# Kernel optimization log

Measured on AMD Instinct MI355X. Metric: run time of the kernel, lower is better.

Reference implementation:

```python
import jax, jax.numpy as jnp
import numpy as np
from jax import lax

L = 6        # n_layers
C = 192      # hidden_channels
FC = 768     # filter_channels
H = 2        # n_heads
DK = C // H  # k_channels per head
K = 3        # ffn kernel_size
W = 4        # window_size
B = 4
T = 2048
EPS = 1e-5


def setup_inputs() -> dict:
    key = jax.random.key(0)
    ks = jax.random.split(key, 16)
    def rn(k, shape, scale):
        return jax.random.normal(k, shape, dtype=jnp.float32) * scale
    xavier = (2.0 / (C + C)) ** 0.5
    return {
        "x": jax.random.normal(ks[0], (B, C, T), dtype=jnp.float32),
        "x_mask": jnp.ones((B, 1, T), dtype=jnp.float32),
        "wq": rn(ks[1], (L, C, C), xavier), "bq": jnp.zeros((L, C), jnp.float32),
        "wk": rn(ks[2], (L, C, C), xavier), "bk": jnp.zeros((L, C), jnp.float32),
        "wv": rn(ks[3], (L, C, C), xavier), "bv": jnp.zeros((L, C), jnp.float32),
        "wo": rn(ks[4], (L, C, C), xavier), "bo": jnp.zeros((L, C), jnp.float32),
        "rel_k": rn(ks[5], (L, 1, 2 * W + 1, DK), DK ** -0.5),
        "rel_v": rn(ks[6], (L, 1, 2 * W + 1, DK), DK ** -0.5),
        "ln1_g": jnp.ones((L, C), jnp.float32), "ln1_b": jnp.zeros((L, C), jnp.float32),
        "ffn_w1": rn(ks[7], (L, FC, C, K), 0.02), "ffn_b1": jnp.zeros((L, FC), jnp.float32),
        "ffn_w2": rn(ks[8], (L, C, FC, K), 0.02), "ffn_b2": jnp.zeros((L, C), jnp.float32),
        "ln2_g": jnp.ones((L, C), jnp.float32), "ln2_b": jnp.zeros((L, C), jnp.float32),
    }


def _layer_norm_ch(x, g, b):
    # normalize over channel dim (axis=1) of [B, C, T]
    m = jnp.mean(x, axis=1, keepdims=True)
    v = jnp.mean((x - m) ** 2, axis=1, keepdims=True)
    return g[None, :, None] * (x - m) * lax.rsqrt(v + EPS) + b[None, :, None]


def _conv1x1(x, w, b):
    return jnp.einsum('oc,bct->bot', w, x) + b[None, :, None]


def _conv1d(x, w, b, pad):
    y = lax.conv_general_dilated(x, w, window_strides=(1,), padding=[(pad, pad)],
                                 dimension_numbers=('NCH', 'OIH', 'NCH'))
    return y + b[None, :, None]


def _get_rel(emb, length):
    # emb: [1, 2W+1, DK] -> [1, 2*length-1, DK]
    pad_len = max(length - (W + 1), 0)
    start = max(W + 1 - length, 0)
    emb = jnp.pad(emb, ((0, 0), (pad_len, pad_len), (0, 0)))
    return emb[:, start:start + 2 * length - 1]


def _rel_to_abs(x):
    # [B, H, L, 2L-1] -> [B, H, L, L]
    b, h, l, _ = x.shape
    x = jnp.pad(x, ((0, 0), (0, 0), (0, 0), (0, 1)))
    x = x.reshape(b, h, l * 2 * l)
    x = jnp.pad(x, ((0, 0), (0, 0), (0, l - 1)))
    return x.reshape(b, h, l + 1, 2 * l - 1)[:, :, :l, l - 1:]


def _abs_to_rel(x):
    # [B, H, L, L] -> [B, H, L, 2L-1]
    b, h, l, _ = x.shape
    x = jnp.pad(x, ((0, 0), (0, 0), (0, 0), (0, l - 1)))
    x = x.reshape(b, h, l * (2 * l - 1))
    x = jnp.pad(x, ((0, 0), (0, 0), (l, 0)))
    return x.reshape(b, h, l, 2 * l)[:, :, :, 1:]


def reference(x, x_mask, wq, bq, wk, bk, wv, bv, wo, bo, rel_k, rel_v,
              ln1_g, ln1_b, ffn_w1, ffn_b1, ffn_w2, ffn_b2, ln2_g, ln2_b):
    attn_mask = x_mask[:, :, None, :] * x_mask[:, :, :, None]  # [B,1,T,T]
    x = x * x_mask
    scale = DK ** -0.5
    pad = (K - 1) // 2
    for l in range(L):
        residual = x
        q = _conv1x1(x, wq[l], bq[l]).reshape(B, H, DK, T).transpose(0, 1, 3, 2)
        k = _conv1x1(x, wk[l], bk[l]).reshape(B, H, DK, T).transpose(0, 1, 3, 2)
        v = _conv1x1(x, wv[l], bv[l]).reshape(B, H, DK, T).transpose(0, 1, 3, 2)
        qs = q * scale
        scores = jnp.einsum('bhtd,bhsd->bhts', qs, k)
        rk = _get_rel(rel_k[l], T)[0]  # [2T-1, DK], heads shared
        scores = scores + _rel_to_abs(jnp.einsum('bhtd,md->bhtm', qs, rk))
        scores = jnp.where(attn_mask == 0, jnp.float32(-1e4), scores)
        p = jax.nn.softmax(scores, axis=-1)
        out = jnp.einsum('bhts,bhsd->bhtd', p, v)
        rv = _get_rel(rel_v[l], T)[0]
        out = out + jnp.einsum('bhtm,md->bhtd', _abs_to_rel(p), rv)
        out = out.transpose(0, 1, 3, 2).reshape(B, C, T)
        out = _conv1x1(out, wo[l], bo[l])
        x = _layer_norm_ch(residual + out, ln1_g[l], ln1_b[l])
        residual = x
        h = _conv1d(x * x_mask, ffn_w1[l], ffn_b1[l], pad)
        h = jax.nn.relu(h)  # activation != 'gelu'
        h = _conv1d(h, ffn_w2[l], ffn_b2[l], pad)
        h = h * x_mask
        x = _layer_norm_ch(residual + h, ln2_g[l], ln2_b[l])
    return x * x_mask
```

## Files before the change

kernel.cpp:

```cpp
#include <hip/hip_runtime.h>

#define LNUM 6
#define CH 192
#define FCH 768
#define NH 2
#define DKH 96
#define WIN 4
#define BATCH 4
#define TLEN 2048
#define EPSV 1e-5f
#define SCH 4
#define CHUNK (TLEN / SCH)
#define NBCT (BATCH*CH*TLEN)
#define NBFT (BATCH*FCH*TLEN)
#define BHT (BATCH*NH*TLEN)

typedef __attribute__((ext_vector_type(8))) short bf16x8;
typedef __attribute__((ext_vector_type(4))) float f32x4;
typedef __attribute__((ext_vector_type(8))) unsigned short u16x8;

__device__ __forceinline__ unsigned short f2bf(float f) {
  unsigned int u = __builtin_bit_cast(unsigned int, f);
  u = (u + 0x7fffu + ((u >> 16) & 1u)) >> 16;
  return (unsigned short)u;
}
__device__ __forceinline__ float bf2f(unsigned short s) {
  return __builtin_bit_cast(float, ((unsigned int)s) << 16);
}
__device__ __forceinline__ float exp2a(float x) {
#if __has_builtin(__builtin_amdgcn_exp2f)
  return __builtin_amdgcn_exp2f(x);
#else
  return exp2f(x);
#endif
}

__global__ __launch_bounds__(256) void prep_all(
    const float* __restrict__ wq, const float* __restrict__ wk, const float* __restrict__ wv,
    const float* __restrict__ bq, const float* __restrict__ bk, const float* __restrict__ bv,
    const float* __restrict__ wo, const float* __restrict__ fw1, const float* __restrict__ fw2,
    unsigned short* __restrict__ Wqkv, float* __restrict__ Bqkv,
    unsigned short* __restrict__ Wob, unsigned short* __restrict__ W1b,
    unsigned short* __restrict__ W2b)
{
  const float qscale = 0.10206207261596575f * 1.4426950408889634f;
  const int n0 = LNUM * 576 * CH;
  const int n1 = LNUM * CH * CH;
  const int n2 = LNUM * 3 * FCH * CH;
  const int n3 = LNUM * 3 * CH * FCH;
  int total = n0 + n1 + n2 + n3;
  for (int i = blockIdx.x * 256 + threadIdx.x; i < total; i += gridDim.x * 256) {
    if (i < n0) {
      int c = i % CH; int n = (i / CH) % 576; int l = i / (CH * 576);
      float sc = (n < 192) ? qscale : 1.f;
      const float* src = (n < 192) ? wq : (n < 384) ? wk : wv;
      int nn = n % 192;
      Wqkv[i] = f2bf(src[((size_t)l * CH + nn) * CH + c] * sc);
      if (c == 0) {
        const float* bs = (n < 192) ? bq : (n < 384) ? bk : bv;
        Bqkv[l * 576 + n] = bs[l * CH + nn] * sc;
      }
    } else if (i < n0 + n1) {
      int j = i - n0;
      Wob[j] = f2bf(wo[j]);
    } else if (i < n0 + n1 + n2) {
      int j = i - n0 - n1;
      int c = j % CH; int t1 = j / CH;
      int f = t1 % FCH; int t2 = t1 / FCH;
      int kk = t2 % 3; int l = t2 / 3;
      W1b[j] = f2bf(fw1[(((size_t)l * FCH + f) * CH + c) * 3 + kk]);
    } else {
      int j = i - n0 - n1 - n2;
      int c = j % FCH; int t1 = j / FCH;
      int f = t1 % CH; int t2 = t1 / CH;
      int kk = t2 % 3; int l = t2 / 3;
      W2b[j] = f2bf(fw2[(((size_t)l * CH + f) * FCH + c) * 3 + kk]);
    }
  }
}

__global__ __launch_bounds__(256) void tin_kernel(const float* __restrict__ x,
    const float* __restrict__ mask, float* __restrict__ Xc, unsigned short* __restrict__ Xbf) {
  __shared__ float ls[32][33];
  int b = blockIdx.z; int c0 = blockIdx.y * 32, t0 = blockIdx.x * 32;
  int tx = threadIdx.x & 31, ty = threadIdx.x >> 5;
  #pragma unroll
  for (int j = 0; j < 4; ++j)
    ls[ty + j * 8][tx] = x[((size_t)b * CH + c0 + ty + j * 8) * TLEN + t0 + tx];
  __syncthreads();
  #pragma unroll
  for (int j = 0; j < 4; ++j) {
    int t = t0 + ty + j * 8;
    float v = ls[tx][ty + j * 8] * mask[b * TLEN + t];
    size_t o = ((size_t)b * TLEN + t) * CH + c0 + tx;
    Xc[o] = v; Xbf[o] = f2bf(v);
  }
}

__global__ __launch_bounds__(256) void tout_kernel(const float* __restrict__ Xc,
    const float* __restrict__ mask, float* __restrict__ out) {
  __shared__ float ls[32][33];
  int b = blockIdx.z; int c0 = blockIdx.y * 32, t0 = blockIdx.x * 32;
  int tx = threadIdx.x & 31, ty = threadIdx.x >> 5;
  #pragma unroll
  for (int j = 0; j < 4; ++j)
    ls[ty + j * 8][tx] = Xc[((size_t)b * TLEN + t0 + ty + j * 8) * CH + c0 + tx];
  __syncthreads();
  #pragma unroll
  for (int j = 0; j < 4; ++j)
    out[((size_t)b * CH + c0 + ty + j * 8) * TLEN + t0 + tx] =
        ls[tx][ty + j * 8] * mask[b * TLEN + t0 + tx];
}

template<int OUTMODE, int NSHIFT, int RELU, int KSPLIT, int MFR>
__global__ __launch_bounds__(256) void gemm_tc(
    const unsigned short* __restrict__ A, const unsigned short* __restrict__ Bw,
    const float* __restrict__ bias, void* __restrict__ Y, int Cin, int N)
{
  constexpr int HALO = (NSHIFT == 3) ? 1 : 0;
  constexpr int AROWS = MFR * 32 + 2 * HALO;
  constexpr int ACH = (AROWS * 8 + 255) / 256;
  constexpr int BCH = (NSHIFT * 64 * 8) / 256;
  __shared__ __align__(16) unsigned short As[AROWS][72];
  __shared__ __align__(16) unsigned short Bs[NSHIFT][64][72];
  int zz = blockIdx.z;
  int b = zz / KSPLIT, ks = zz % KSPLIT;
  int t0 = blockIdx.x * (MFR * 32), n0 = blockIdx.y * 64;
  int tid = threadIdx.x;
  int w = tid >> 6, lane = tid & 63;
  int wr = w >> 1, wc = w & 1;
  int lr = lane & 15, lg = lane >> 4;
  const unsigned short* Ab = A + (size_t)b * TLEN * Cin;
  int klen = Cin / KSPLIT, k0 = ks * klen;

  int ar[ACH], ac8[ACH]; bool aok[ACH], ain[ACH];
  #pragma unroll
  for (int j = 0; j < ACH; ++j) {
    int f = tid + j * 256;
    ar[j] = f >> 3; ac8[j] = (f & 7) * 8;
    aok[j] = (f < AROWS * 8);
    int tg = t0 - HALO + ar[j];
    ain[j] = aok[j] && (!HALO || (tg >= 0 && tg < TLEN));
  }
  int brr[BCH], bkk[BCH], bc8[BCH];
  #pragma unroll
  for (int j = 0; j < BCH; ++j) {
    int f = tid + j * 256;
    bkk[j] = f >> 9; brr[j] = (f >> 3) & 63; bc8[j] = (f & 7) * 8;
  }

  u16x8 areg[ACH], breg[BCH];
  f32x4 acc[MFR][2] = {};

  #pragma unroll
  for (int j = 0; j < ACH; ++j) {
    u16x8 v = {};
    if (ain[j]) v = *(const u16x8*)&Ab[(size_t)(t0 - HALO + ar[j]) * Cin + k0 + ac8[j]];
    areg[j] = v;
  }
  #pragma unroll
  for (int j = 0; j < BCH; ++j)
    breg[j] = *(const u16x8*)&Bw[((size_t)bkk[j] * N + n0 + brr[j]) * Cin + k0 + bc8[j]];

  for (int kc = k0; kc < k0 + klen; kc += 64) {
    __syncthreads();
    #pragma unroll
    for (int j = 0; j < ACH; ++j)
      if (aok[j]) *(u16x8*)&As[ar[j]][ac8[j]] = areg[j];
    #pragma unroll
    for (int j = 0; j < BCH; ++j)
      *(u16x8*)&Bs[bkk[j]][brr[j]][bc8[j]] = breg[j];
    if (kc + 64 < k0 + klen) {
      int kn = kc + 64;
      #pragma unroll
      for (int j = 0; j < ACH; ++j) {
        u16x8 v = {};
        if (ain[j]) v = *(const u16x8*)&Ab[(size_t)(t0 - HALO + ar[j]) * Cin + kn + ac8[j]];
        areg[j] = v;
      }
      #pragma unroll
      for (int j = 0; j < BCH; ++j)
        breg[j] = *(const u16x8*)&Bw[((size_t)bkk[j] * N + n0 + brr[j]) * Cin + kn + bc8[j]];
    }
    __syncthreads();
    #pragma unroll
    for (int kk = 0; kk < NSHIFT; ++kk) {
      #pragma unroll
      for (int k2 = 0; k2 < 2; ++k2) {
        bf16x8 b0 = *(const bf16x8*)&Bs[kk][wc * 32 + lr][k2 * 32 + lg * 8];
        bf16x8 b1 = *(const bf16x8*)&Bs[kk][wc * 32 + 16 + lr][k2 * 32 + lg * 8];
        #pragma unroll
        for (int i = 0; i < MFR; ++i) {
          bf16x8 a = *(const bf16x8*)&As[wr * MFR * 16 + i * 16 + lr + kk][k2 * 32 + lg * 8];
          acc[i][0] = __builtin_amdgcn_mfma_f32_16x16x32_bf16(a, b0, acc[i][0], 0, 0, 0);
          acc[i][1] = __builtin_amdgcn_mfma_f32_16x16x32_bf16(a, b1, acc[i][1], 0, 0, 0);
        }
      }
    }
  }
  #pragma unroll
  for (int i = 0; i < MFR; ++i) {
    #pragma unroll
    for (int j = 0; j < 2; ++j) {
      int n = n0 + wc * 32 + j * 16 + lr;
      float bb = (ks == 0) ? bias[n] : 0.f;
      float vals[4];
      #pragma unroll
      for (int r = 0; r < 4; ++r) {
        float v = acc[i][j][r] + bb;
        if (RELU) v = fmaxf(v, 0.f);
        vals[r] = v;
      }
      int trow = t0 + wr * MFR * 16 + i * 16 + lg * 4;
      if (OUTMODE == 0) {
        unsigned short* Yp = (unsigned short*)Y + ((size_t)b * TLEN + trow) * N + n;
        #pragma unroll
        for (int r = 0; r < 4; ++r) Yp[(size_t)r * N] = f2bf(vals[r]);
      } else {
        unsigned short* base = (unsigned short*)Y;
        if (n0 < 192) {
          unsigned short* Yp = base + ((size_t)b * TLEN + trow) * CH + n;
          #pragma unroll
          for (int r = 0; r < 4; ++r) Yp[(size_t)r * CH] = f2bf(vals[r]);
        } else if (n0 < 384) {
          unsigned short* Yp = base + (size_t)NBCT + ((size_t)b * TLEN + trow) * CH + (n - 192);
          #pragma unroll
          for (int r = 0; r < 4; ++r) Yp[(size_t)r * CH] = f2bf(vals[r]);
        } else {
          ushort4 pk;
          pk.x = f2bf(vals[0]); pk.y = f2bf(vals[1]); pk.z = f2bf(vals[2]); pk.w = f2bf(vals[3]);
          *(ushort4*)(base + 2 * (size_t)NBCT + ((size_t)b * CH + (n - 384)) * TLEN + trow) = pk;
        }
      }
    }
  }
}

__global__ __launch_bounds__(256) void ln_cl_kernel(
    const float* __restrict__ res, const unsigned short* __restrict__ yb,
    const float* __restrict__ g, const float* __restrict__ bt,
    float* __restrict__ Xc, unsigned short* __restrict__ Xbf)
{
  int row = blockIdx.x * 4 + (threadIdx.x >> 6);
  int lane = threadIdx.x & 63;
  const float* r = res + (size_t)row * CH;
  const unsigned short* y = yb + (size_t)row * CH;
  float v[3]; float s = 0.f, s2 = 0.f;
  #pragma unroll
  for (int j = 0; j < 3; ++j) {
    float t = r[lane + 64 * j] + bf2f(y[lane + 64 * j]);
    v[j] = t; s += t; s2 += t * t;
  }
  #pragma unroll
  for (int m = 1; m <= 32; m <<= 1) {
    s += __shfl_xor(s, m, 64);
    s2 += __shfl_xor(s2, m, 64);
  }
  float mean = s * (1.f / CH);
  float var = s2 * (1.f / CH) - mean * mean;
  float rs = rsqrtf(var + EPSV);
  #pragma unroll
  for (int j = 0; j < 3; ++j) {
    int c = lane + 64 * j;
    float o = g[c] * (v[j] - mean) * rs + bt[c];
    size_t idx = (size_t)row * CH + c;
    Xc[idx] = o; Xbf[idx] = f2bf(o);
  }
}

__global__ __launch_bounds__(256, 4) void flash_part(
    const unsigned short* __restrict__ Qg, const unsigned short* __restrict__ Kg,
    const unsigned short* __restrict__ Vg, const float* __restrict__ relk,
    float* __restrict__ Opart, float* __restrict__ mG, float* __restrict__ lG,
    float* __restrict__ bandG)
{
  __shared__ __align__(16) unsigned short KsB[64 * 104];
  __shared__ __align__(16) unsigned short QV[96 * 72];
  __shared__ float qrk[64][9];
  int bh = blockIdx.y; int b = bh >> 1, h = bh & 1;
  int t0 = blockIdx.x * 64;
  int c0 = blockIdx.z * CHUNK;
  int tid = threadIdx.x; int w = tid >> 6, lane = tid & 63;
  int lr = lane & 15, lg = lane >> 4;
  int q = w * 16 + lr;
  const unsigned short* Qb = Qg + (size_t)b * TLEN * CH + h * DKH;
  const unsigned short* Kb = Kg + (size_t)b * TLEN * CH + h * DKH;
  const unsigned short* Vb = Vg + ((size_t)b * CH + h * DKH) * TLEN;
  unsigned short (*Qs)[104] = (unsigned short(*)[104])QV;
  unsigned short (*Vs)[72] = (unsigned short(*)[72])QV;
  unsigned short (*Ks)[104] = (unsigned short(*)[104])KsB;
  unsigned short (*Ps)[72] = (unsigned short(*)[72])KsB;

  int kr[3], kc8[3], vr[3], vc8[3];
  #pragma unroll
  for (int j = 0; j < 3; ++j) {
    int f = tid + j * 256;
    kr[j] = f / 12; kc8[j] = (f % 12) * 8;
    vr[j] = f >> 3; vc8[j] = (f & 7) * 8;
  }

  for (int f = tid; f < 64 * 12; f += 256) {
    int r = f / 12, c8 = (f % 12) * 8;
    *(u16x8*)&Qs[r][c8] = *(const u16x8*)&Qb[(size_t)(t0 + r) * CH + c8];
  }
  __syncthreads();
  bool overlap = (t0 + 64 + WIN > c0) && (t0 - WIN < c0 + CHUNK);
  if (overlap) {
    for (int f = tid; f < 576; f += 256) {
      int r = f / 9, dd = f - (f / 9) * 9;
      float s = 0.f;
      #pragma unroll 8
      for (int d = 0; d < DKH; ++d) s += bf2f(Qs[r][d]) * relk[dd * DKH + d];
      qrk[r][dd] = s;
    }
  }
  bf16x8 qf[3];
  #pragma unroll
  for (int kc = 0; kc < 3; ++kc) qf[kc] = *(const bf16x8*)&Qs[q][kc * 32 + lg * 8];
  float mrow = -1e30f, lrow = 0.f;
  f32x4 oacc[6] = {};

  u16x8 kreg[3], vreg[3];
  #pragma unroll
  for (int j = 0; j < 3; ++j)
    kreg[j] = *(const u16x8*)&Kb[(size_t)(c0 + kr[j]) * CH + kc8[j]];
  #pragma unroll
  for (int j = 0; j < 3; ++j)
    vreg[j] = *(const u16x8*)&Vb[(size_t)vr[j] * TLEN + c0 + vc8[j]];

  for (int it = 0; it < CHUNK / 64; ++it) {
    int s0 = c0 + it * 64;
    __syncthreads();
    #pragma unroll
    for (int j = 0; j < 3; ++j) *(u16x8*)&Ks[kr[j]][kc8[j]] = kreg[j];
    #pragma unroll
    for (int j = 0; j < 3; ++j) *(u16x8*)&Vs[vr[j]][vc8[j]] = vreg[j];
    if (it + 1 < CHUNK / 64) {
      int sn = s0 + 64;
      #pragma unroll
      for (int j = 0; j < 3; ++j)
        kreg[j] = *(const u16x8*)&Kb[(size_t)(sn + kr[j]) * CH + kc8[j]];
      #pragma unroll
      for (int j = 0; j < 3; ++j)
        vreg[j] = *(const u16x8*)&Vb[(size_t)vr[j] * TLEN + sn + vc8[j]];
    }
    __syncthreads();

    f32x4 sacc[4] = {};
    __builtin_amdgcn_s_setprio(1);
    #pragma unroll
    for (int kc = 0; kc < 3; ++kc) {
      #pragma unroll
      for (int ct = 0; ct < 4; ++ct) {
        bf16x8 kfr = *(const bf16x8*)&Ks[ct * 16 + lr][kc * 32 + lg * 8];
        sacc[ct] = __builtin_amdgcn_mfma_f32_16x16x32_bf16(kfr, qf[kc], sacc[ct], 0, 0, 0);
      }
    }
    __builtin_amdgcn_s_setprio(0);
    if (s0 + 64 + WIN > t0 && s0 < t0 + 64 + WIN) {
      #pragma unroll
      for (int ct = 0; ct < 4; ++ct)
        #pragma unroll
        for (int r = 0; r < 4; ++r) {
          int dlt = (s0 + ct * 16 + lg * 4 + r) - (t0 + q);
          if (dlt >= -WIN && dlt <= WIN) {
            float v = sacc[ct][r] + qrk[q][dlt + WIN];
            sacc[ct][r] = v;
            bandG[((size_t)bh * TLEN + t0 + q) * 9 + dlt + WIN] = v;
          }
        }
    }
    float cm[4];
    #pragma unroll
    for (int ct = 0; ct < 4; ++ct)
      cm[ct] = fmaxf(fmaxf(sacc[ct][0], sacc[ct][1]), fmaxf(sacc[ct][2], sacc[ct][3]));
    float tmax = fmaxf(fmaxf(cm[0], cm[1]), fmaxf(cm[2], cm[3]));
    tmax = fmaxf(tmax, __shfl_xor(tmax, 16, 64));
    tmax = fmaxf(tmax, __shfl_xor(tmax, 32, 64));
    bool upd = !__all(tmax <= mrow + 8.f);
    float mnew = upd ? fmaxf(mrow, tmax) : mrow;
    float psum = 0.f;
    ushort4 pk[4];
    #pragma unroll
    for (int ct = 0; ct < 4; ++ct) {
      float p0 = exp2a(sacc[ct][0] - mnew), p1 = exp2a(sacc[ct][1] - mnew);
      float p2 = exp2a(sacc[ct][2] - mnew), p3 = exp2a(sacc[ct][3] - mnew);
      psum += (p0 + p1) + (p2 + p3);
      pk[ct].x = f2bf(p0); pk[ct].y = f2bf(p1); pk[ct].z = f2bf(p2); pk[ct].w = f2bf(p3);
    }
    if (upd) {
      float alpha = exp2a(mrow - mnew);
      lrow *= alpha;
      float alo[4];
      #pragma unroll
      for (int r = 0; r < 4; ++r) alo[r] = __shfl(alpha, lg * 4 + r, 64);
      #pragma unroll
      for (int dt = 0; dt < 6; ++dt)
        #pragma unroll
        for (int r = 0; r < 4; ++r) oacc[dt][r] *= alo[r];
      mrow = mnew;
    }
    lrow += psum;
    __syncthreads();
    #pragma unroll
    for (int ct = 0; ct < 4; ++ct)
      *(ushort4*)&Ps[q][ct * 16 + lg * 4] = pk[ct];
    __builtin_amdgcn_s_setprio(1);
    #pragma unroll
    for (int ks = 0; ks < 2; ++ks) {
      bf16x8 pa = *(const bf16x8*)&Ps[q][ks * 32 + lg * 8];
      #pragma unroll
      for (int dt = 0; dt < 6; ++dt) {
        bf16x8 vf = *(const bf16x8*)&Vs[dt * 16 + lr][ks * 32 + lg * 8];
        oacc[dt] = __builtin_amdgcn_mfma_f32_16x16x32_bf16(pa, vf, oacc[dt], 0, 0, 0);
      }
    }
    __builtin_amdgcn_s_setprio(0);
  }

  size_t pbase = ((size_t)blockIdx.z * (BATCH * NH) + bh) * TLEN + t0;
  #pragma unroll
  for (int dt = 0; dt < 6; ++dt)
    #pragma unroll
    for (int r = 0; r < 4; ++r)
      Opart[(pbase + w * 16 + lg * 4 + r) * 96 + dt * 16 + lr] = oacc[dt][r];
  float lfull = lrow;
  lfull += __shfl_xor(lfull, 16, 64);
  lfull += __shfl_xor(lfull, 32, 64);
  if (lg == 0) {
    mG[pbase + q] = mrow;
    lG[pbase + q] = lfull;
  }
}

__global__ __launch_bounds__(256) void flash_combine(
    const float* __restrict__ Opart, const float* __restrict__ mG,
    const float* __restrict__ lG, const float* __restrict__ bandG,
    const float* __restrict__ relv, unsigned short* __restrict__ AO)
{
  int sub = threadIdx.x >> 7;
  int d = threadIdx.x & 127;
  int row = blockIdx.x * 2 + sub;
  int bh = row >> 11, t = row & 2047;
  float mv[SCH], lv[SCH], m = -1e30f;
  #pragma unroll
  for (int c = 0; c < SCH; ++c) {
    mv[c] = mG[(size_t)c * BHT + row];
    lv[c] = lG[(size_t)c * BHT + row];
    m = fmaxf(m, mv[c]);
  }
  float L = 0.f, e[SCH];
  #pragma unroll
  for (int c = 0; c < SCH; ++c) { e[c] = exp2a(mv[c] - m); L += lv[c] * e[c]; }
  if (d < 96) {
    float acc = 0.f;
    #pragma unroll
    for (int c = 0; c < SCH; ++c)
      acc += Opart[((size_t)c * BHT + row) * 96 + d] * e[c];
    #pragma unroll
    for (int dd = 0; dd < 9; ++dd) {
      int s = t + dd - WIN;
      if (s >= 0 && s < TLEN)
        acc += exp2a(bandG[(size_t)row * 9 + dd] - m) * relv[dd * 96 + d];
    }
    int b = bh >> 1, h = bh & 1;
    AO[((size_t)b * TLEN + t) * CH + h * DKH + d] = f2bf(acc / L);
  }
}

extern "C" void kernel_launch(void* const* d_in, const int* in_sizes, int n_in,
                              void* d_out, int out_size, void* d_ws, size_t ws_size,
                              hipStream_t stream) {
  (void)in_sizes; (void)n_in; (void)out_size; (void)ws_size;
  const float* x    = (const float*)d_in[0];
  const float* mask = (const float*)d_in[1];
  const float* wq   = (const float*)d_in[2];
  const float* bq   = (const float*)d_in[3];
  const float* wk   = (const float*)d_in[4];
  const float* bk   = (const float*)d_in[5];
  const float* wv   = (const float*)d_in[6];
  const float* bv   = (const float*)d_in[7];
  const float* wo   = (const float*)d_in[8];
  const float* bo   = (const float*)d_in[9];
  const float* relk = (const float*)d_in[10];
  const float* relv = (const float*)d_in[11];
  const float* ln1g = (const float*)d_in[12];
  const float* ln1b = (const float*)d_in[13];
  const float* fw1  = (const float*)d_in[14];
  const float* fb1  = (const float*)d_in[15];
  const float* fw2  = (const float*)d_in[16];
  const float* fb2  = (const float*)d_in[17];
  const float* ln2g = (const float*)d_in[18];
  const float* ln2b = (const float*)d_in[19];

  char* p = (char*)d_ws;
  float* Xc = (float*)p;                      p += (size_t)NBCT * 4;
  unsigned short* Xbf  = (unsigned short*)p;  p += (size_t)NBCT * 2;
  unsigned short* Qbf  = (unsigned short*)p;  p += (size_t)NBCT * 2;
  unsigned short* Kbf  = (unsigned short*)p;  p += (size_t)NBCT * 2;
  unsigned short* Vbf  = (unsigned short*)p;  p += (size_t)NBCT * 2;
  unsigned short* AObf = (unsigned short*)p;  p += (size_t)NBCT * 2;
  char* R = p;                                p += (size_t)NBCT * 16;
  float* Opart = (float*)R;
  unsigned short* Ybf = (unsigned short*)R;
  unsigned short* Hbf = (unsigned short*)(R + (size_t)NBCT * 2);
  float* mG = (float*)p;                      p += (size_t)SCH * BHT * 4;
  float* lG = (float*)p;                      p += (size_t)SCH * BHT * 4;
  float* bandG = (float*)p;                   p += (size_t)BHT * 9 * 4;
  unsigned short* Wqkv = (unsigned short*)p;  p += (size_t)LNUM * 576 * CH * 2;
  float* Bqkv = (float*)p;                    p += (size_t)LNUM * 576 * 4;
  unsigned short* Wob  = (unsigned short*)p;  p += (size_t)LNUM * CH * CH * 2;
  unsigned short* W1b  = (unsigned short*)p;  p += (size_t)LNUM * 3 * FCH * CH * 2;
  unsigned short* W2b  = (unsigned short*)p;

  prep_all<<<2048, 256, 0, stream>>>(wq, wk, wv, bq, bk, bv, wo, fw1, fw2,
                                     Wqkv, Bqkv, Wob, W1b, W2b);
  tin_kernel<<<dim3(TLEN / 32, CH / 32, BATCH), 256, 0, stream>>>(x, mask, Xc, Xbf);

  for (int l = 0; l < LNUM; ++l) {
    gemm_tc<3, 1, 0, 1, 4><<<dim3(16, 9, 4), 256, 0, stream>>>(
        Xbf, Wqkv + (size_t)l * 576 * CH, Bqkv + l * 576, Qbf, CH, 576);
    flash_part<<<dim3(32, 8, SCH), 256, 0, stream>>>(
        Qbf, Kbf, Vbf, relk + (size_t)l * 9 * DKH, Opart, mG, lG, bandG);
    flash_combine<<<BHT / 2, 256, 0, stream>>>(
        Opart, mG, lG, bandG, relv + (size_t)l * 9 * DKH, AObf);
    gemm_tc<0, 1, 0, 1, 1><<<dim3(64, 3, 4), 256, 0, stream>>>(
        AObf, Wob + (size_t)l * CH * CH, bo + l * CH, Ybf, CH, CH);
    ln_cl_kernel<<<BATCH * TLEN / 4, 256, 0, stream>>>(
        Xc, Ybf, ln1g + l * CH, ln1b + l * CH, Xc, Xbf);
    gemm_tc<0, 3, 1, 1, 4><<<dim3(16, 12, 4), 256, 0, stream>>>(
        Xbf, W1b + (size_t)l * 3 * FCH * CH, fb1 + l * FCH, Hbf, CH, FCH);
    gemm_tc<0, 3, 0, 1, 2><<<dim3(32, 3, 4), 256, 0, stream>>>(
        Hbf, W2b + (size_t)l * 3 * CH * FCH, fb2 + l * CH, Ybf, FCH, CH);
    ln_cl_kernel<<<BATCH * TLEN / 4, 256, 0, stream>>>(
        Xc, Ybf, ln2g + l * CH, ln2b + l * CH, Xc, Xbf);
  }
  tout_kernel<<<dim3(TLEN / 32, CH / 32, BATCH), 256, 0, stream>>>(Xc, mask, (float*)d_out);
}
```

Measured before the change: 664.6 us.

## Fuse output projection with residual add and layer norm; flatten flash grid

Adds a gemm_woln kernel that computes the attention output projection for 16-row tiles covering all 192 channels, then applies bias, the residual add and the channel layer norm in its epilogue, writing both fp32 and bf16 activations. This replaces a separate GEMM plus LN kernel and removes the Ybf round trip through global memory and one launch per layer. Separately, flash_part switches to a 1D grid with bh as the fastest-varying index, which changes block scheduling order and may improve K/V cache locality. The fused GEMM has small tiles and reloads the full weight per block, which may lower MFMA efficiency.

```diff
diff --git a/kernel.cpp b/kernel.cpp
--- a/kernel.cpp
+++ b/kernel.cpp
@@ -236,6 +236,104 @@
   }
 }
 
+__global__ __launch_bounds__(256) void gemm_woln(
+    const unsigned short* __restrict__ A, const unsigned short* __restrict__ Bw,
+    const float* __restrict__ bias, const float* __restrict__ g,
+    const float* __restrict__ bt, float* __restrict__ Xc, unsigned short* __restrict__ Xbf)
+{
+  __shared__ __align__(16) unsigned short As[16][72];
+  __shared__ __align__(16) unsigned short Bs[192][72];
+  __shared__ float sred[4][16][2];
+  int b = blockIdx.y;
+  int t0 = blockIdx.x * 16;
+  int tid = threadIdx.x;
+  int w = tid >> 6, lane = tid & 63;
+  int lr = lane & 15, lg = lane >> 4;
+  const unsigned short* Ab = A + (size_t)b * TLEN * CH;
+  bool aok = tid < 128;
+  int ar = tid >> 3, ac8 = (tid & 7) * 8;
+  int brr[6], bc8[6];
+  #pragma unroll
+  for (int j = 0; j < 6; ++j) { int f = tid + j * 256; brr[j] = f >> 3; bc8[j] = (f & 7) * 8; }
+
+  u16x8 areg = {}; u16x8 breg[6];
+  f32x4 acc[3] = {};
+  if (aok) areg = *(const u16x8*)&Ab[(size_t)(t0 + ar) * CH + ac8];
+  #pragma unroll
+  for (int j = 0; j < 6; ++j)
+    breg[j] = *(const u16x8*)&Bw[(size_t)brr[j] * CH + bc8[j]];
+
+  for (int kc = 0; kc < CH; kc += 64) {
+    __syncthreads();
+    if (aok) *(u16x8*)&As[ar][ac8] = areg;
+    #pragma unroll
+    for (int j = 0; j < 6; ++j) *(u16x8*)&Bs[brr[j]][bc8[j]] = breg[j];
+    if (kc + 64 < CH) {
+      int kn = kc + 64;
+      if (aok) areg = *(const u16x8*)&Ab[(size_t)(t0 + ar) * CH + kn + ac8];
+      #pragma unroll
+      for (int j = 0; j < 6; ++j)
+        breg[j] = *(const u16x8*)&Bw[(size_t)brr[j] * CH + kn + bc8[j]];
+    }
+    __syncthreads();
+    #pragma unroll
+    for (int k2 = 0; k2 < 2; ++k2) {
+      bf16x8 a = *(const bf16x8*)&As[lr][k2 * 32 + lg * 8];
+      #pragma unroll
+      for (int j = 0; j < 3; ++j) {
+        bf16x8 bfr = *(const bf16x8*)&Bs[w * 48 + j * 16 + lr][k2 * 32 + lg * 8];
+        acc[j] = __builtin_amdgcn_mfma_f32_16x16x32_bf16(a, bfr, acc[j], 0, 0, 0);
+      }
+    }
+  }
+  float vv[3][4], sp[4] = {}, sp2[4] = {};
+  #pragma unroll
+  for (int j = 0; j < 3; ++j) {
+    int col = w * 48 + j * 16 + lr;
+    float bb = bias[col];
+    #pragma unroll
+    for (int r = 0; r < 4; ++r) {
+      int row = t0 + lg * 4 + r;
+      float y = acc[j][r] + bb;
+      float res = Xc[((size_t)b * TLEN + row) * CH + col];
+      float t = res + y;
+      vv[j][r] = t; sp[r] += t; sp2[r] += t * t;
+    }
+  }
+  #pragma unroll
+  for (int m = 1; m <= 8; m <<= 1)
+    #pragma unroll
+    for (int r = 0; r < 4; ++r) {
+      sp[r] += __shfl_xor(sp[r], m, 64);
+      sp2[r] += __shfl_xor(sp2[r], m, 64);
+    }
+  __syncthreads();
+  if (lr == 0) {
+    #pragma unroll
+    for (int r = 0; r < 4; ++r) {
+      sred[w][lg * 4 + r][0] = sp[r];
+      sred[w][lg * 4 + r][1] = sp2[r];
+    }
+  }
+  __syncthreads();
+  #pragma unroll
+  for (int r = 0; r < 4; ++r) {
+    int row = lg * 4 + r;
+    float s  = sred[0][row][0] + sred[1][row][0] + sred[2][row][0] + sred[3][row][0];
+    float s2 = sred[0][row][1] + sred[1][row][1] + sred[2][row][1] + sred[3][row][1];
+    float mean = s * (1.f / CH);
+    float var = s2 * (1.f / CH) - mean * mean;
+    float rs = rsqrtf(var + EPSV);
+    #pragma unroll
+    for (int j = 0; j < 3; ++j) {
+      int col = w * 48 + j * 16 + lr;
+      float o = g[col] * (vv[j][r] - mean) * rs + bt[col];
+      size_t idx = ((size_t)b * TLEN + t0 + row) * CH + col;
+      Xc[idx] = o; Xbf[idx] = f2bf(o);
+    }
+  }
+}
+
 __global__ __launch_bounds__(256) void ln_cl_kernel(
     const float* __restrict__ res, const unsigned short* __restrict__ yb,
     const float* __restrict__ g, const float* __restrict__ bt,
@@ -277,9 +375,13 @@
   __shared__ __align__(16) unsigned short KsB[64 * 104];
   __shared__ __align__(16) unsigned short QV[96 * 72];
   __shared__ float qrk[64][9];
-  int bh = blockIdx.y; int b = bh >> 1, h = bh & 1;
-  int t0 = blockIdx.x * 64;
-  int c0 = blockIdx.z * CHUNK;
+  int id = blockIdx.x;
+  int bh = id & 7;
+  int rest = id >> 3;
+  int t0 = (rest & 31) * 64;
+  int zc = rest >> 5;
+  int c0 = zc * CHUNK;
+  int b = bh >> 1, h = bh & 1;
   int tid = threadIdx.x; int w = tid >> 6, lane = tid & 63;
   int lr = lane & 15, lg = lane >> 4;
   int q = w * 16 + lr;
@@ -418,7 +520,7 @@
     __builtin_amdgcn_s_setprio(0);
   }
 
-  size_t pbase = ((size_t)blockIdx.z * (BATCH * NH) + bh) * TLEN + t0;
+  size_t pbase = ((size_t)zc * (BATCH * NH) + bh) * TLEN + t0;
   #pragma unroll
   for (int dt = 0; dt < 6; ++dt)
     #pragma unroll
@@ -520,14 +622,13 @@
   for (int l = 0; l < LNUM; ++l) {
     gemm_tc<3, 1, 0, 1, 4><<<dim3(16, 9, 4), 256, 0, stream>>>(
         Xbf, Wqkv + (size_t)l * 576 * CH, Bqkv + l * 576, Qbf, CH, 576);
-    flash_part<<<dim3(32, 8, SCH), 256, 0, stream>>>(
+    flash_part<<<dim3(32 * 8 * SCH), 256, 0, stream>>>(
         Qbf, Kbf, Vbf, relk + (size_t)l * 9 * DKH, Opart, mG, lG, bandG);
     flash_combine<<<BHT / 2, 256, 0, stream>>>(
         Opart, mG, lG, bandG, relv + (size_t)l * 9 * DKH, AObf);
-    gemm_tc<0, 1, 0, 1, 1><<<dim3(64, 3, 4), 256, 0, stream>>>(
-        AObf, Wob + (size_t)l * CH * CH, bo + l * CH, Ybf, CH, CH);
-    ln_cl_kernel<<<BATCH * TLEN / 4, 256, 0, stream>>>(
-        Xc, Ybf, ln1g + l * CH, ln1b + l * CH, Xc, Xbf);
+    gemm_woln<<<dim3(TLEN / 16, BATCH), 256, 0, stream>>>(
+        AObf, Wob + (size_t)l * CH * CH, bo + l * CH,
+        ln1g + l * CH, ln1b + l * CH, Xc, Xbf);
     gemm_tc<0, 3, 1, 1, 4><<<dim3(16, 12, 4), 256, 0, stream>>>(
         Xbf, W1b + (size_t)l * 3 * FCH * CH, fb1 + l * FCH, Hbf, CH, FCH);
     gemm_tc<0, 3, 0, 1, 2><<<dim3(32, 3, 4), 256, 0, stream>>>(
```

Measured after the change: 652.7 us. About the same (-1.8%).
